# Optimization experiments

Hardware: AMD Instinct MI355X
Metric: run time of the kernel (lower is better)

Reference implementation:

```python
import jax, jax.numpy as jnp
import numpy as np

NUM_HEADS = 8


def _xavier_uniform(key, shape):
    fan_in, fan_out = shape[0], shape[1]
    a = np.sqrt(6.0 / (fan_in + fan_out))
    return jax.random.uniform(key, shape, jnp.float32, -a, a)


def setup_inputs() -> dict:
    key = jax.random.key(0)
    ks = jax.random.split(key, 8)
    B, N = 4, 1024
    input_dim, num_gru_units, output_dim = 1, 64, 64
    D = input_dim + num_gru_units  # 65
    F = output_dim // NUM_HEADS  # 8 per-head features

    inputs = jax.random.normal(ks[0], (B, N, input_dim), jnp.float32)
    hidden_state = jax.random.normal(ks[1], (B, N, num_gru_units), jnp.float32)

    # random sparse binary adjacency with self-loops
    adj_np = (np.asarray(jax.random.uniform(ks[2], (N, N))) < 0.03).astype(np.float32)
    np.fill_diagonal(adj_np, 1.0)
    adj_mask = jnp.asarray(adj_np)

    # calculate_laplacian_with_self_loop: D^{-1/2} (A + I) D^{-1/2}
    a_hat = adj_np + np.eye(N, dtype=np.float32)
    deg = a_hat.sum(axis=1)
    d_inv_sqrt = 1.0 / np.sqrt(deg)
    laplacian = jnp.asarray((a_hat * d_inv_sqrt[:, None]) * d_inv_sqrt[None, :])

    W = _xavier_uniform(ks[3], (D, F * NUM_HEADS))
    attn = _xavier_uniform(ks[4], (2 * F, 1))
    weights = jax.random.normal(ks[5], (D, output_dim), jnp.float32)
    biases = jax.random.normal(ks[6], (output_dim,), jnp.float32)

    return {"inputs": inputs, "hidden_state": hidden_state, "W": W,
            "attn": attn, "weights": weights, "biases": biases,
            "adj_mask": adj_mask, "laplacian": laplacian}


def reference(inputs, hidden_state, W, attn, weights, biases, adj_mask, laplacian):
    # concat inputs and GRU hidden state: [B, N, D]
    h = jnp.concatenate([inputs, hidden_state], axis=-1)
    B, N, D = h.shape
    H = NUM_HEADS
    F = W.shape[1] // H

    # --- GAT branch ---
    ht = (h @ W).reshape(B, N, H, F)  # [B, N, H, F]
    # concat([h_i, h_j]) @ attn == h_i @ attn[:F] + h_j @ attn[F:]
    a_src = attn[:F, 0]
    a_dst = attn[F:, 0]
    e_src = jnp.einsum('bnhf,f->bnh', ht, a_src)  # [B, N, H]
    e_dst = jnp.einsum('bnhf,f->bnh', ht, a_dst)  # [B, N, H]
    e = e_src[:, :, None, :] + e_dst[:, None, :, :]  # [B, N_i, N_j, H]
    e = jax.nn.leaky_relu(e, negative_slope=0.2)
    e = jnp.where(adj_mask[None, :, :, None] == 0, -1.0e9, e)
    att = jax.nn.softmax(e, axis=2)  # softmax over neighbor j (dropout off: eval)
    gat_out = jnp.einsum('bijh,bjhf->bihf', att, ht).reshape(B, N, H * F)

    # --- Laplacian GCN branch ---
    a_times_concat = jnp.einsum('ij,bjd->bid', laplacian, h)  # [B, N, D]
    lap_out = a_times_concat @ weights + biases  # [B, N, output_dim]

    # fusion == 'concat'
    return jnp.concatenate([gat_out, lap_out], axis=-1)
```

## Files before the change

kernel.cpp:

```cpp
#include <hip/hip_runtime.h>


#define NN 1024
typedef unsigned long long u64;

__global__ __launch_bounds__(256) void fused_one(
    const float* __restrict__ adj,
    const float* __restrict__ lap,
    const float* __restrict__ inp,
    const float* __restrict__ hid,
    const float* __restrict__ W,
    const float* __restrict__ W2,
    const float* __restrict__ attnv,
    const float* __restrict__ biases,
    float* __restrict__ out)
{
    __shared__ float wsrc_s[520];
    __shared__ float wdstT_s[8][68];
    __shared__ float stash[4][2][8][68];
    __shared__ float ps_s[4][8][8];
    __shared__ int   idx_s[4][64];
    __shared__ float lapv_s[4][64];
    __shared__ float aggX[4][8][68];
    __shared__ float lapX[4][68];
    __shared__ float den_s[4][8];
    __shared__ float es_s[4][8];

    const int tid  = threadIdx.x;
    const int wid  = tid >> 6;
    const int lane = tid & 63;
    const int row  = blockIdx.x * 4 + wid;
    const int b    = row >> 10;
    const int i    = row & (NN - 1);
    const int brow = b << 10;

    for (int e = tid; e < 520; e += 256) {
        const int hh = e / 65, k = e - hh * 65;
        const int dr = (k < 64) ? (k + 1) : 0;
        float s2 = 0.f;
        #pragma unroll
        for (int f = 0; f < 8; ++f)
            s2 = fmaf(W[dr * 64 + hh * 8 + f], attnv[8 + f], s2);
        wdstT_s[hh][k] = s2;
    }
    for (int e = tid; e < 520; e += 256) {
        const int d = e >> 3, hh = e & 7;
        float s1 = 0.f;
        #pragma unroll
        for (int f = 0; f < 8; ++f)
            s1 = fmaf(W[d * 64 + hh * 8 + f], attnv[f], s1);
        wsrc_s[e] = s1;
    }

    idx_s[wid][lane]  = i;
    lapv_s[wid][lane] = 0.f;
    int c;
    {
        const float4* arow = (const float4*)(adj + i * NN);
        const float4* lrow = (const float4*)(lap + i * NN);
        float4 a[4], l[4];
        #pragma unroll
        for (int it = 0; it < 4; ++it) a[it] = arow[it * 64 + lane];
        #pragma unroll
        for (int it = 0; it < 4; ++it) l[it] = lrow[it * 64 + lane];
        const u64 lt = (1ull << lane) - 1ull;
        int base = 0;
        #pragma unroll
        for (int it = 0; it < 4; ++it) {
            const bool m0 = a[it].x != 0.f, m1 = a[it].y != 0.f,
                       m2 = a[it].z != 0.f, m3 = a[it].w != 0.f;
            const u64 b0 = __ballot(m0), b1 = __ballot(m1),
                      b2 = __ballot(m2), b3 = __ballot(m3);
            int pos = base + __popcll(b0 & lt) + __popcll(b1 & lt)
                           + __popcll(b2 & lt) + __popcll(b3 & lt);
            const int j0 = it * 256 + lane * 4;
            if (m0 && pos < 64) { idx_s[wid][pos] = j0;   lapv_s[wid][pos] = l[it].x; ++pos; }
            if (m1 && pos < 64) { idx_s[wid][pos] = j0+1; lapv_s[wid][pos] = l[it].y; ++pos; }
            if (m2 && pos < 64) { idx_s[wid][pos] = j0+2; lapv_s[wid][pos] = l[it].z; ++pos; }
            if (m3 && pos < 64) { idx_s[wid][pos] = j0+3; lapv_s[wid][pos] = l[it].w; }
            base += __popcll(b0) + __popcll(b1) + __popcll(b2) + __popcll(b3);
        }
        c = (base < 64) ? base : 64;
    }

    __syncthreads();

    const int h  = lane >> 3;
    const int dg = lane & 7;
    const int n8 = lane >> 3;
    const int hB = lane & 7;

    {
        float e = 0.f;
        #pragma unroll
        for (int t = 0; t < 9; ++t) {
            const int d = dg + 8 * t;
            float v = 0.f, w = 0.f;
            if (d == 0)       v = inp[row];
            else if (d <= 64) v = hid[row * 64 + d - 1];
            if (d <= 64)      w = wsrc_s[d * 8 + h];
            e = fmaf(v, w, e);
        }
        e += __shfl_xor(e, 1); e += __shfl_xor(e, 2); e += __shfl_xor(e, 4);
        if (dg == 0) es_s[wid][h] = e;
    }

    const int   j_lane = idx_s[wid][lane];
    const int   nch    = (c + 7) >> 3;
    const float w0dst  = wdstT_s[hB][64];

    float agg[8];
    #pragma unroll
    for (int t = 0; t < 8; ++t) agg[t] = 0.f;
    float lapa = 0.f, den_p = 0.f, a0 = 0.f, l0 = 0.f;

    float vstA[8];
    #pragma unroll
    for (int n = 0; n < 8; ++n)
        vstA[n] = hid[(u64)(brow | __shfl(j_lane, n)) * 64 + lane];
    #pragma unroll
    for (int n = 0; n < 8; ++n) stash[wid][0][n][lane] = vstA[n];

    int cur = 0;
    for (int g = 0; g < nch; ++g) {
        const int   jv   = idx_s[wid][g * 8 + n8];
        const float lv_v = lapv_s[wid][g * 8 + n8];
        const float in_v = inp[brow | jv];

        float vst[8];
        if (g + 1 < nch) {
            #pragma unroll
            for (int n = 0; n < 8; ++n)
                vst[n] = hid[(u64)(brow | __shfl(j_lane, (g + 1) * 8 + n)) * 64 + lane];
        }

        {
            const float4* srow = (const float4*)&stash[wid][cur][n8][0];
            const float4* wrow = (const float4*)&wdstT_s[hB][0];
            float acc0 = 0.f, acc1 = 0.f;
            #pragma unroll
            for (int q = 0; q < 16; q += 2) {
                const float4 s0 = srow[q],     w0 = wrow[q];
                const float4 s1 = srow[q + 1], w1 = wrow[q + 1];
                acc0 = fmaf(s0.x, w0.x, acc0); acc0 = fmaf(s0.y, w0.y, acc0);
                acc0 = fmaf(s0.z, w0.z, acc0); acc0 = fmaf(s0.w, w0.w, acc0);
                acc1 = fmaf(s1.x, w1.x, acc1); acc1 = fmaf(s1.y, w1.y, acc1);
                acc1 = fmaf(s1.z, w1.z, acc1); acc1 = fmaf(s1.w, w1.w, acc1);
            }
            const float ed = fmaf(in_v, w0dst, acc0 + acc1);
            float s = es_s[wid][hB] + ed;
            s = (s > 0.f) ? s : 0.2f * s;
            const int kk = g * 8 + n8;
            const float p = (kk < c) ? __expf(s) : 0.f;
            ps_s[wid][n8][hB] = p;
            den_p += p;
            a0 = fmaf(p, in_v, a0);
            l0 = fmaf(lv_v, in_v, l0);
        }

        #pragma unroll
        for (int e = 0; e < 8; ++e) {
            const float  v   = stash[wid][cur][e][lane];
            const float4 pa  = *(const float4*)&ps_s[wid][e][0];
            const float4 pb  = *(const float4*)&ps_s[wid][e][4];
            const float  lvn = lapv_s[wid][g * 8 + e];
            agg[0] = fmaf(pa.x, v, agg[0]); agg[1] = fmaf(pa.y, v, agg[1]);
            agg[2] = fmaf(pa.z, v, agg[2]); agg[3] = fmaf(pa.w, v, agg[3]);
            agg[4] = fmaf(pb.x, v, agg[4]); agg[5] = fmaf(pb.y, v, agg[5]);
            agg[6] = fmaf(pb.z, v, agg[6]); agg[7] = fmaf(pb.w, v, agg[7]);
            lapa   = fmaf(lvn, v, lapa);
        }

        if (g + 1 < nch) {
            #pragma unroll
            for (int n = 0; n < 8; ++n) stash[wid][cur ^ 1][n][lane] = vst[n];
        }
        cur ^= 1;
    }

    den_p += __shfl_xor(den_p, 8); den_p += __shfl_xor(den_p, 16); den_p += __shfl_xor(den_p, 32);
    a0    += __shfl_xor(a0, 8);    a0    += __shfl_xor(a0, 16);    a0    += __shfl_xor(a0, 32);
    l0    += __shfl_xor(l0, 8);    l0    += __shfl_xor(l0, 16);    l0    += __shfl_xor(l0, 32);
    if (lane < 8) {
        den_s[wid][lane]     = den_p;
        aggX[wid][lane][64]  = a0;
    }
    if (lane == 0) lapX[wid][64] = l0;

    #pragma unroll
    for (int hh = 0; hh < 8; ++hh) aggX[wid][hh][lane] = agg[hh];
    lapX[wid][lane] = lapa;

    float accg = 0.f, accl = 0.f;
    #pragma unroll 4
    for (int q = 0; q < 16; ++q) {
        const float4 ag = *(const float4*)&aggX[wid][h][4 * q];
        const float4 lp = *(const float4*)&lapX[wid][4 * q];
        accg = fmaf(ag.x, W [(4*q + 1) * 64 + lane], accg);
        accg = fmaf(ag.y, W [(4*q + 2) * 64 + lane], accg);
        accg = fmaf(ag.z, W [(4*q + 3) * 64 + lane], accg);
        accg = fmaf(ag.w, W [(4*q + 4) * 64 + lane], accg);
        accl = fmaf(lp.x, W2[(4*q + 1) * 64 + lane], accl);
        accl = fmaf(lp.y, W2[(4*q + 2) * 64 + lane], accl);
        accl = fmaf(lp.z, W2[(4*q + 3) * 64 + lane], accl);
        accl = fmaf(lp.w, W2[(4*q + 4) * 64 + lane], accl);
    }
    accg = fmaf(aggX[wid][h][64], W [lane], accg);
    accl = fmaf(lapX[wid][64],    W2[lane], accl);

    const float den = den_s[wid][h];
    out[row * 128 + lane]      = accg / den;
    out[row * 128 + 64 + lane] = accl + biases[lane];
}

extern "C" void kernel_launch(void* const* d_in, const int* in_sizes, int n_in,
                              void* d_out, int out_size, void* d_ws, size_t ws_size,
                              hipStream_t stream) {
    const float* inp    = (const float*)d_in[0];
    const float* hid    = (const float*)d_in[1];
    const float* W      = (const float*)d_in[2];
    const float* attnv  = (const float*)d_in[3];
    const float* W2     = (const float*)d_in[4];
    const float* biases = (const float*)d_in[5];
    const float* adj    = (const float*)d_in[6];
    const float* lap    = (const float*)d_in[7];
    float* out = (float*)d_out;

    fused_one<<<NN, 256, 0, stream>>>(
        adj, lap, inp, hid, W, W2, attnv, biases, out);
}
```

Before: 28.59 us.

## Share adjacency scan across batches and split neighbor chunks over two waves

Each block now handles one node i for all four batches with 512 threads. The adjacency and Laplacian row is scanned once by a single wave instead of four times. Each batch's neighbor chunks are split between two waves that interleave even and odd chunks, and their partial sums are combined through shared memory before the projection. The weight precompute runs on another wave group at the same time as the scan. Per-neighbor inp and Laplacian values now come from register shuffles. The cost is an extra block barrier and a reduction step, and each wave's in-loop double buffering is replaced by a single stash.

Measured after the change: 38.12 us. 33.3% more time.

```diff
diff --git a/kernel.cpp b/kernel.cpp
--- a/kernel.cpp
+++ b/kernel.cpp
@@ -4,7 +4,7 @@
 #define NN 1024
 typedef unsigned long long u64;
 
-__global__ __launch_bounds__(256) void fused_one(
+__global__ __launch_bounds__(512) void fused_one(
     const float* __restrict__ adj,
     const float* __restrict__ lap,
     const float* __restrict__ inp,
@@ -17,45 +17,27 @@
 {
     __shared__ float wsrc_s[520];
     __shared__ float wdstT_s[8][68];
-    __shared__ float stash[4][2][8][68];
-    __shared__ float ps_s[4][8][8];
-    __shared__ int   idx_s[4][64];
-    __shared__ float lapv_s[4][64];
+    __shared__ float stash[8][8][68];
+    __shared__ float ps_s[8][8][8];
+    __shared__ int   idx_s[64];
+    __shared__ float lapv_s[64];
     __shared__ float aggX[4][8][68];
     __shared__ float lapX[4][68];
-    __shared__ float den_s[4][8];
-    __shared__ float es_s[4][8];
+    __shared__ float denX[4][8];
+    __shared__ int   cnt_sh;
 
     const int tid  = threadIdx.x;
     const int wid  = tid >> 6;
     const int lane = tid & 63;
-    const int row  = blockIdx.x * 4 + wid;
-    const int b    = row >> 10;
-    const int i    = row & (NN - 1);
+    const int b    = wid & 3;
+    const int par  = wid >> 2;
+    const int i    = blockIdx.x;
     const int brow = b << 10;
-
-    for (int e = tid; e < 520; e += 256) {
-        const int hh = e / 65, k = e - hh * 65;
-        const int dr = (k < 64) ? (k + 1) : 0;
-        float s2 = 0.f;
-        #pragma unroll
-        for (int f = 0; f < 8; ++f)
-            s2 = fmaf(W[dr * 64 + hh * 8 + f], attnv[8 + f], s2);
-        wdstT_s[hh][k] = s2;
-    }
-    for (int e = tid; e < 520; e += 256) {
-        const int d = e >> 3, hh = e & 7;
-        float s1 = 0.f;
-        #pragma unroll
-        for (int f = 0; f < 8; ++f)
-            s1 = fmaf(W[d * 64 + hh * 8 + f], attnv[f], s1);
-        wsrc_s[e] = s1;
-    }
-
-    idx_s[wid][lane]  = i;
-    lapv_s[wid][lane] = 0.f;
-    int c;
-    {
+    const int row  = brow | i;
+
+    if (wid == 0) {
+        idx_s[lane]  = i;
+        lapv_s[lane] = 0.f;
         const float4* arow = (const float4*)(adj + i * NN);
         const float4* lrow = (const float4*)(lap + i * NN);
         float4 a[4], l[4];
@@ -74,68 +56,92 @@
             int pos = base + __popcll(b0 & lt) + __popcll(b1 & lt)
                            + __popcll(b2 & lt) + __popcll(b3 & lt);
             const int j0 = it * 256 + lane * 4;
-            if (m0 && pos < 64) { idx_s[wid][pos] = j0;   lapv_s[wid][pos] = l[it].x; ++pos; }
-            if (m1 && pos < 64) { idx_s[wid][pos] = j0+1; lapv_s[wid][pos] = l[it].y; ++pos; }
-            if (m2 && pos < 64) { idx_s[wid][pos] = j0+2; lapv_s[wid][pos] = l[it].z; ++pos; }
-            if (m3 && pos < 64) { idx_s[wid][pos] = j0+3; lapv_s[wid][pos] = l[it].w; }
+            if (m0 && pos < 64) { idx_s[pos] = j0;   lapv_s[pos] = l[it].x; ++pos; }
+            if (m1 && pos < 64) { idx_s[pos] = j0+1; lapv_s[pos] = l[it].y; ++pos; }
+            if (m2 && pos < 64) { idx_s[pos] = j0+2; lapv_s[pos] = l[it].z; ++pos; }
+            if (m3 && pos < 64) { idx_s[pos] = j0+3; lapv_s[pos] = l[it].w; }
             base += __popcll(b0) + __popcll(b1) + __popcll(b2) + __popcll(b3);
         }
-        c = (base < 64) ? base : 64;
+        if (lane == 0) cnt_sh = (base < 64) ? base : 64;
+    } else if (par == 1) {
+        for (int e = tid - 256; e < 520; e += 256) {
+            const int hh = e / 65, k = e - hh * 65;
+            const int dr = (k < 64) ? (k + 1) : 0;
+            float s2 = 0.f;
+            #pragma unroll
+            for (int f = 0; f < 8; ++f)
+                s2 = fmaf(W[dr * 64 + hh * 8 + f], attnv[8 + f], s2);
+            wdstT_s[hh][k] = s2;
+        }
+        for (int e = tid - 256; e < 520; e += 256) {
+            const int d = e >> 3, hh = e & 7;
+            float s1 = 0.f;
+            #pragma unroll
+            for (int f = 0; f < 8; ++f)
+                s1 = fmaf(W[d * 64 + hh * 8 + f], attnv[f], s1);
+            wsrc_s[e] = s1;
+        }
     }
 
     __syncthreads();
 
-    const int h  = lane >> 3;
-    const int dg = lane & 7;
+    const int c   = cnt_sh;
+    const int nch = (c + 7) >> 3;
+
+    const int   j_all  = idx_s[lane];
+    const float lv_all = lapv_s[lane];
+    const float in_all = inp[brow | j_all];
+
     const int n8 = lane >> 3;
     const int hB = lane & 7;
 
+    float es_red;
     {
+        const int dg_ = lane & 7, h_ = lane >> 3;
         float e = 0.f;
         #pragma unroll
         for (int t = 0; t < 9; ++t) {
-            const int d = dg + 8 * t;
+            const int d = dg_ + 8 * t;
             float v = 0.f, w = 0.f;
             if (d == 0)       v = inp[row];
             else if (d <= 64) v = hid[row * 64 + d - 1];
-            if (d <= 64)      w = wsrc_s[d * 8 + h];
+            if (d <= 64)      w = wsrc_s[d * 8 + h_];
             e = fmaf(v, w, e);
         }
         e += __shfl_xor(e, 1); e += __shfl_xor(e, 2); e += __shfl_xor(e, 4);
-        if (dg == 0) es_s[wid][h] = e;
-    }
-
-    const int   j_lane = idx_s[wid][lane];
-    const int   nch    = (c + 7) >> 3;
-    const float w0dst  = wdstT_s[hB][64];
+        es_red = e;
+    }
+    const float es_B  = __shfl(es_red, (lane & 7) << 3);
+    const float w0dst = wdstT_s[hB][64];
 
     float agg[8];
     #pragma unroll
     for (int t = 0; t < 8; ++t) agg[t] = 0.f;
     float lapa = 0.f, den_p = 0.f, a0 = 0.f, l0 = 0.f;
 
-    float vstA[8];
-    #pragma unroll
-    for (int n = 0; n < 8; ++n)
-        vstA[n] = hid[(u64)(brow | __shfl(j_lane, n)) * 64 + lane];
-    #pragma unroll
-    for (int n = 0; n < 8; ++n) stash[wid][0][n][lane] = vstA[n];
-
-    int cur = 0;
-    for (int g = 0; g < nch; ++g) {
-        const int   jv   = idx_s[wid][g * 8 + n8];
-        const float lv_v = lapv_s[wid][g * 8 + n8];
-        const float in_v = inp[brow | jv];
-
+    if (par < nch) {
         float vst[8];
-        if (g + 1 < nch) {
+        #pragma unroll
+        for (int n = 0; n < 8; ++n)
+            vst[n] = hid[(u64)(brow | __shfl(j_all, par * 8 + n)) * 64 + lane];
+        #pragma unroll
+        for (int n = 0; n < 8; ++n) stash[wid][n][lane] = vst[n];
+    }
+
+    for (int g = par; g < nch; g += 2) {
+        const bool more = (g + 2 < nch);
+        float vnx[8];
+        if (more) {
             #pragma unroll
             for (int n = 0; n < 8; ++n)
-                vst[n] = hid[(u64)(brow | __shfl(j_lane, (g + 1) * 8 + n)) * 64 + lane];
-        }
+                vnx[n] = hid[(u64)(brow | __shfl(j_all, (g + 2) * 8 + n)) * 64 + lane];
+        }
+
+        const float in_v = __shfl(in_all, g * 8 + n8);
+        const float lv_v = __shfl(lv_all, g * 8 + n8);
 
         {
-            const float4* srow = (const float4*)&stash[wid][cur][n8][0];
+            const float4* srow = (const float4*)&stash[wid][n8][0];
             const float4* wrow = (const float4*)&wdstT_s[hB][0];
             float acc0 = 0.f, acc1 = 0.f;
             #pragma unroll
@@ -148,7 +154,7 @@
                 acc1 = fmaf(s1.z, w1.z, acc1); acc1 = fmaf(s1.w, w1.w, acc1);
             }
             const float ed = fmaf(in_v, w0dst, acc0 + acc1);
-            float s = es_s[wid][hB] + ed;
+            float s = es_B + ed;
             s = (s > 0.f) ? s : 0.2f * s;
             const int kk = g * 8 + n8;
             const float p = (kk < c) ? __expf(s) : 0.f;
@@ -160,10 +166,10 @@
 
         #pragma unroll
         for (int e = 0; e < 8; ++e) {
-            const float  v   = stash[wid][cur][e][lane];
+            const float  v   = stash[wid][e][lane];
             const float4 pa  = *(const float4*)&ps_s[wid][e][0];
             const float4 pb  = *(const float4*)&ps_s[wid][e][4];
-            const float  lvn = lapv_s[wid][g * 8 + e];
+            const float  lvn = __shfl(lv_all, g * 8 + e);
             agg[0] = fmaf(pa.x, v, agg[0]); agg[1] = fmaf(pa.y, v, agg[1]);
             agg[2] = fmaf(pa.z, v, agg[2]); agg[3] = fmaf(pa.w, v, agg[3]);
             agg[4] = fmaf(pb.x, v, agg[4]); agg[5] = fmaf(pb.y, v, agg[5]);
@@ -171,46 +177,57 @@
             lapa   = fmaf(lvn, v, lapa);
         }
 
-        if (g + 1 < nch) {
-            #pragma unroll
-            for (int n = 0; n < 8; ++n) stash[wid][cur ^ 1][n][lane] = vst[n];
-        }
-        cur ^= 1;
+        if (more) {
+            #pragma unroll
+            for (int n = 0; n < 8; ++n) stash[wid][n][lane] = vnx[n];
+        }
     }
 
     den_p += __shfl_xor(den_p, 8); den_p += __shfl_xor(den_p, 16); den_p += __shfl_xor(den_p, 32);
     a0    += __shfl_xor(a0, 8);    a0    += __shfl_xor(a0, 16);    a0    += __shfl_xor(a0, 32);
     l0    += __shfl_xor(l0, 8);    l0    += __shfl_xor(l0, 16);    l0    += __shfl_xor(l0, 32);
-    if (lane < 8) {
-        den_s[wid][lane]     = den_p;
-        aggX[wid][lane][64]  = a0;
-    }
-    if (lane == 0) lapX[wid][64] = l0;
-
-    #pragma unroll
-    for (int hh = 0; hh < 8; ++hh) aggX[wid][hh][lane] = agg[hh];
-    lapX[wid][lane] = lapa;
-
-    float accg = 0.f, accl = 0.f;
-    #pragma unroll 4
-    for (int q = 0; q < 16; ++q) {
-        const float4 ag = *(const float4*)&aggX[wid][h][4 * q];
-        const float4 lp = *(const float4*)&lapX[wid][4 * q];
-        accg = fmaf(ag.x, W [(4*q + 1) * 64 + lane], accg);
-        accg = fmaf(ag.y, W [(4*q + 2) * 64 + lane], accg);
-        accg = fmaf(ag.z, W [(4*q + 3) * 64 + lane], accg);
-        accg = fmaf(ag.w, W [(4*q + 4) * 64 + lane], accg);
-        accl = fmaf(lp.x, W2[(4*q + 1) * 64 + lane], accl);
-        accl = fmaf(lp.y, W2[(4*q + 2) * 64 + lane], accl);
-        accl = fmaf(lp.z, W2[(4*q + 3) * 64 + lane], accl);
-        accl = fmaf(lp.w, W2[(4*q + 4) * 64 + lane], accl);
-    }
-    accg = fmaf(aggX[wid][h][64], W [lane], accg);
-    accl = fmaf(lapX[wid][64],    W2[lane], accl);
-
-    const float den = den_s[wid][h];
-    out[row * 128 + lane]      = accg / den;
-    out[row * 128 + 64 + lane] = accl + biases[lane];
+
+    if (par == 1) {
+        #pragma unroll
+        for (int hh = 0; hh < 8; ++hh) aggX[b][hh][lane] = agg[hh];
+        lapX[b][lane] = lapa;
+        if (lane < 8) { denX[b][lane] = den_p; aggX[b][lane][64] = a0; }
+        if (lane == 0) lapX[b][64] = l0;
+    }
+    __syncthreads();
+
+    if (par == 0) {
+        #pragma unroll
+        for (int hh = 0; hh < 8; ++hh)
+            aggX[b][hh][lane] += agg[hh];
+        lapX[b][lane] += lapa;
+        if (lane < 8) aggX[b][lane][64] += a0;
+        if (lane == 0) lapX[b][64] += l0;
+
+        const float denc = den_p + denX[b][lane & 7];
+
+        const int h = lane >> 3;
+        float accg = 0.f, accl = 0.f;
+        #pragma unroll 4
+        for (int q = 0; q < 16; ++q) {
+            const float4 ag = *(const float4*)&aggX[b][h][4 * q];
+            const float4 lp = *(const float4*)&lapX[b][4 * q];
+            accg = fmaf(ag.x, W [(4*q + 1) * 64 + lane], accg);
+            accg = fmaf(ag.y, W [(4*q + 2) * 64 + lane], accg);
+            accg = fmaf(ag.z, W [(4*q + 3) * 64 + lane], accg);
+            accg = fmaf(ag.w, W [(4*q + 4) * 64 + lane], accg);
+            accl = fmaf(lp.x, W2[(4*q + 1) * 64 + lane], accl);
+            accl = fmaf(lp.y, W2[(4*q + 2) * 64 + lane], accl);
+            accl = fmaf(lp.z, W2[(4*q + 3) * 64 + lane], accl);
+            accl = fmaf(lp.w, W2[(4*q + 4) * 64 + lane], accl);
+        }
+        accg = fmaf(aggX[b][h][64], W [lane], accg);
+        accl = fmaf(lapX[b][64],    W2[lane], accl);
+
+        const float den = __shfl(denc, h);
+        out[row * 128 + lane]      = accg / den;
+        out[row * 128 + 64 + lane] = accl + biases[lane];
+    }
 }
 
 extern "C" void kernel_launch(void* const* d_in, const int* in_sizes, int n_in,
@@ -226,6 +243,6 @@
     const float* lap    = (const float*)d_in[7];
     float* out = (float*)d_out;
 
-    fused_one<<<NN, 256, 0, stream>>>(
+    fused_one<<<NN, 512, 0, stream>>>(
         adj, lap, inp, hid, W, W2, attnv, biases, out);
 }
```
